# Optimization experiments

Hardware: AMD Instinct MI355X
Metric: run time of the kernel (lower is better)

Reference implementation:

```python
import jax, jax.numpy as jnp
import numpy as np

WS = 8            # window size
N = WS * WS       # tokens per window
C = 192           # in_features
H = 6             # heads
HD = C // H       # head dim
MH = 256          # meta network hidden
BW = 4096         # batch_size * windows
NW_MASK = 64      # number of mask window patterns


def _relative_coords_log():
    idx = np.arange(WS)
    coords = np.stack(np.meshgrid(idx, idx, indexing='ij'), axis=0).reshape(2, -1)  # [2, N]
    rel = coords[:, :, None] - coords[:, None, :]            # [2, N, N]
    rel = rel.transpose(1, 2, 0).reshape(-1, 2).astype(np.float32)  # [N*N, 2]
    return jnp.asarray(np.sign(rel) * np.log1p(np.abs(rel)))


def setup_inputs() -> dict:
    key = jax.random.key(0)
    ks = jax.random.split(key, 12)
    s = 0.02
    return {
        'x': jax.random.normal(ks[0], (BW, C, WS, WS), jnp.float32),
        'mask': jax.random.normal(ks[1], (NW_MASK, N, N), jnp.float32),
        'W_qkv': jax.random.normal(ks[2], (C, 3 * C), jnp.float32) * s,
        'b_qkv': jnp.zeros((3 * C,), jnp.float32),
        'W_proj': jax.random.normal(ks[3], (C, C), jnp.float32) * s,
        'b_proj': jnp.zeros((C,), jnp.float32),
        'mW1': jax.random.normal(ks[4], (2, MH), jnp.float32) * 0.1,
        'mb1': jnp.zeros((MH,), jnp.float32),
        'mW2': jax.random.normal(ks[5], (MH, H), jnp.float32) * 0.1,
        'mb2': jnp.zeros((H,), jnp.float32),
        'tau': jnp.ones((H,), jnp.float32),
    }


def _l2norm(v):
    n = jnp.sqrt(jnp.sum(v * v, axis=-1, keepdims=True))
    return v / jnp.maximum(n, 1e-12)


def reference(x, mask, W_qkv, b_qkv, W_proj, b_proj, mW1, mb1, mW2, mb2, tau):
    Bw = x.shape[0]
    # [Bw, C, ws, ws] -> tokens [Bw, N, C]
    tokens = x.reshape(Bw, C, N).transpose(0, 2, 1)
    qkv = tokens @ W_qkv + b_qkv                                  # [Bw, N, 3C]
    qkv = qkv.reshape(Bw, N, 3, H, HD).transpose(2, 0, 3, 1, 4)   # [3, Bw, H, N, HD]
    q, k, v = qkv[0], qkv[1], qkv[2]
    # scaled cosine attention
    attn = jnp.einsum('bhnd,bhmd->bhnm', _l2norm(q), _l2norm(k))
    attn = attn / jnp.clip(tau, 0.01, None)[None, :, None, None]
    # continuous relative position bias via meta network
    rel_log = _relative_coords_log()                              # [N*N, 2]
    bias = jax.nn.relu(rel_log @ mW1 + mb1) @ mW2 + mb2           # [N*N, H]
    bias = bias.T.reshape(H, N, N)
    attn = attn + bias[None]
    # shifted-window mask, pattern indexed by window id modulo nW_mask
    idx = jnp.arange(Bw) % mask.shape[0]
    attn = attn + mask[idx][:, None]                              # [Bw, 1, N, N]
    attn = jax.nn.softmax(attn, axis=-1)
    out = jnp.einsum('bhnm,bhmd->bhnd', attn, v)
    out = out.transpose(0, 2, 1, 3).reshape(Bw, N, C)
    out = out @ W_proj + b_proj
    # back to [Bw, C, ws, ws]
    return out.transpose(0, 2, 1).reshape(Bw, C, WS, WS)
```

## Files before the change

### kernel.cpp

```cpp
#include <hip/hip_runtime.h>

typedef _Float16 f16;
typedef _Float16 f16x2 __attribute__((ext_vector_type(2)));
typedef _Float16 f16x4 __attribute__((ext_vector_type(4)));
typedef _Float16 f16x8 __attribute__((ext_vector_type(8)));
typedef float f32x4 __attribute__((ext_vector_type(4)));

#define NT 64
#define CH 192
#define NH 6
#define MH 256
#define BWIN 4096
#define LOG2E 1.44269504f

#define STOK 200
#define SMEM_FUSED 49152
#define SMEM_SPLIT 25600

#define MFMA16(a, b, c) __builtin_amdgcn_mfma_f32_16x16x16f16(a, b, c, 0, 0, 0)
#define MFMA32(a, b, c) __builtin_amdgcn_mfma_f32_16x16x32_f16(a, b, c, 0, 0, 0)

__device__ __forceinline__ int qkidx(int n, int d) {
    return n * 32 + ((((d >> 3) + (n >> 1)) & 3) << 3) + (d & 7);
}

__global__ void bias_kernel(const float* __restrict__ mW1, const float* __restrict__ mb1,
                            const float* __restrict__ mW2, const float* __restrict__ mb2,
                            float* __restrict__ bias_tbl) {
    int p = blockIdx.x * blockDim.x + threadIdx.x;
    if (p >= NT * NT) return;
    int n = p >> 6, m = p & 63;
    float di = (float)((n >> 3) - (m >> 3));
    float dj = (float)((n & 7) - (m & 7));
    float r0 = copysignf(log1pf(fabsf(di)), di);
    float r1 = copysignf(log1pf(fabsf(dj)), dj);
    float acc[NH];
#pragma unroll
    for (int h = 0; h < NH; h++) acc[h] = mb2[h];
    for (int k = 0; k < MH; k++) {
        float hv = fmaxf(r0 * mW1[k] + r1 * mW1[MH + k] + mb1[k], 0.0f);
#pragma unroll
        for (int h = 0; h < NH; h++) acc[h] += hv * mW2[k * NH + h];
    }
#pragma unroll
    for (int h = 0; h < NH; h++) bias_tbl[h * (NT * NT) + p] = acc[h];
}

__global__ void prep_kernel(const float* __restrict__ Wqkv, const float* __restrict__ Wproj,
                            f16* __restrict__ Wpk, f16* __restrict__ Wpp) {
    int i = blockIdx.x * blockDim.x + threadIdx.x;
    const int NQ = 36 * 6 * 64 * 8;
    if (i < NQ) {
        int t = i & 7, lane = (i >> 3) & 63, ks = (i >> 9) % 6, ct = i >> 9; ct /= 6;
        int o = 16 * ct + (lane & 15);
        int c = ks * 32 + (lane >> 4) * 8 + t;
        Wpk[i] = (f16)Wqkv[c * 576 + o];
    } else if (i < NQ + 12 * 6 * 64 * 8) {
        int j = i - NQ;
        int t = j & 7, lane = (j >> 3) & 63, ks = (j >> 9) % 6, ct = j >> 9; ct /= 6;
        int o = 16 * ct + (lane & 15);
        int c = ks * 32 + (lane >> 4) * 8 + t;
        Wpp[j] = (f16)Wproj[c * 192 + o];
    }
}

__global__ void comb_kernel(const float* __restrict__ mask, const float* __restrict__ bias_tbl,
                            float* __restrict__ comb) {
    int j = blockIdx.x * blockDim.x + threadIdx.x;
    if (j >= 64 * NH * NT * NT) return;
    int im = j / (NH * NT * NT);
    int rem = j % (NH * NT * NT);
    int h = rem >> 12;
    int p = rem & 4095;
    comb[j] = (mask[im * 4096 + p] + bias_tbl[h * 4096 + p]) * LOG2E;
}

__launch_bounds__(384)
__global__ void qkv_kernel(const float* __restrict__ x, const float* __restrict__ bqkv,
                           const f16* __restrict__ Wpk, f16* __restrict__ qkv_ws) {
    __shared__ __align__(16) f16 tok[NT * STOK];

    const int tid = threadIdx.x;
    const int l   = tid & 63;
    const int w   = __builtin_amdgcn_readfirstlane(tid >> 6);
    const int b   = blockIdx.x;
    const int c16 = l & 15;
    const int g4  = l >> 4;

    {
        const float* xb = x + (size_t)b * (CH * NT);
        const int n4 = 4 * c16;
#pragma unroll
        for (int i = 0; i < 4; i++) {
            int c = 32 * w + 8 * g4 + 2 * i;
            f32x4 a0 = *(const f32x4*)(xb + c * NT + n4);
            f32x4 a1 = *(const f32x4*)(xb + (c + 1) * NT + n4);
#pragma unroll
            for (int j = 0; j < 4; j++) {
                f16x2 p;
                p[0] = (f16)a0[j];
                p[1] = (f16)a1[j];
                *(f16x2*)(tok + (n4 + j) * STOK + c) = p;
            }
        }
    }
    __syncthreads();

    f16* dstq = qkv_ws + (size_t)(b * NH + w) * 6144;
    f16* dstk = dstq + 2048;
    f16* dstv = dstq + 4096;

    {
        f32x4 acc[2][4] = {};
#pragma unroll
        for (int ks = 0; ks < 6; ks++) {
            f16x8 af[4];
#pragma unroll
            for (int nt = 0; nt < 4; nt++)
                af[nt] = *(const f16x8*)(tok + (16 * nt + c16) * STOK + ks * 32 + 8 * g4);
#pragma unroll
            for (int dt = 0; dt < 2; dt++) {
                f16x8 wf = *(const f16x8*)(Wpk + (((size_t)(2 * w + dt) * 6 + ks) * 64 + l) * 8);
#pragma unroll
                for (int nt = 0; nt < 4; nt++)
                    acc[dt][nt] = MFMA32(wf, af[nt], acc[dt][nt]);
            }
        }
        f32x4 bb0 = *(const f32x4*)(bqkv + 32 * w + 4 * g4);
        f32x4 bb1 = *(const f32x4*)(bqkv + 32 * w + 16 + 4 * g4);
#pragma unroll
        for (int nt = 0; nt < 4; nt++) {
            float a0[4], a1[4];
            float ss = 0.f;
#pragma unroll
            for (int r = 0; r < 4; r++) {
                a0[r] = acc[0][nt][r] + bb0[r];
                a1[r] = acc[1][nt][r] + bb1[r];
                ss += a0[r] * a0[r] + a1[r] * a1[r];
            }
            ss += __shfl_xor(ss, 16);
            ss += __shfl_xor(ss, 32);
            float inv = 1.0f / fmaxf(sqrtf(ss), 1e-12f);
            f16x4 h0, h1;
#pragma unroll
            for (int r = 0; r < 4; r++) {
                h0[r] = (f16)(a0[r] * inv);
                h1[r] = (f16)(a1[r] * inv);
            }
            *(f16x4*)(dstq + (16 * nt + c16) * 32 + 4 * g4)      = h0;
            *(f16x4*)(dstq + (16 * nt + c16) * 32 + 16 + 4 * g4) = h1;
        }
    }
    {
        f32x4 acc[2][4] = {};
#pragma unroll
        for (int ks = 0; ks < 6; ks++) {
            f16x8 af[4];
#pragma unroll
            for (int nt = 0; nt < 4; nt++)
                af[nt] = *(const f16x8*)(tok + (16 * nt + c16) * STOK + ks * 32 + 8 * g4);
#pragma unroll
            for (int dt = 0; dt < 2; dt++) {
                f16x8 wf = *(const f16x8*)(Wpk + (((size_t)(12 + 2 * w + dt) * 6 + ks) * 64 + l) * 8);
#pragma unroll
                for (int nt = 0; nt < 4; nt++)
                    acc[dt][nt] = MFMA32(wf, af[nt], acc[dt][nt]);
            }
        }
        f32x4 bb0 = *(const f32x4*)(bqkv + CH + 32 * w + 4 * g4);
        f32x4 bb1 = *(const f32x4*)(bqkv + CH + 32 * w + 16 + 4 * g4);
#pragma unroll
        for (int nt = 0; nt < 4; nt++) {
            float a0[4], a1[4];
            float ss = 0.f;
#pragma unroll
            for (int r = 0; r < 4; r++) {
                a0[r] = acc[0][nt][r] + bb0[r];
                a1[r] = acc[1][nt][r] + bb1[r];
                ss += a0[r] * a0[r] + a1[r] * a1[r];
            }
            ss += __shfl_xor(ss, 16);
            ss += __shfl_xor(ss, 32);
            float inv = 1.0f / fmaxf(sqrtf(ss), 1e-12f);
            f16x4 h0, h1;
#pragma unroll
            for (int r = 0; r < 4; r++) {
                h0[r] = (f16)(a0[r] * inv);
                h1[r] = (f16)(a1[r] * inv);
            }
            *(f16x4*)(dstk + (16 * nt + c16) * 32 + 4 * g4)      = h0;
            *(f16x4*)(dstk + (16 * nt + c16) * 32 + 16 + 4 * g4) = h1;
        }
    }
    {
        f32x4 acc[2][4] = {};
#pragma unroll
        for (int ks = 0; ks < 6; ks++) {
            f16x8 af[4];
#pragma unroll
            for (int mt = 0; mt < 4; mt++)
                af[mt] = *(const f16x8*)(tok + (16 * mt + c16) * STOK + ks * 32 + 8 * g4);
#pragma unroll
            for (int dt = 0; dt < 2; dt++) {
                f16x8 wf = *(const f16x8*)(Wpk + (((size_t)(24 + 2 * w + dt) * 6 + ks) * 64 + l) * 8);
#pragma unroll
                for (int mt = 0; mt < 4; mt++)
                    acc[dt][mt] = MFMA32(af[mt], wf, acc[dt][mt]);
            }
        }
#pragma unroll
        for (int dt = 0; dt < 2; dt++) {
            float bb = bqkv[384 + 32 * w + 16 * dt + c16];
#pragma unroll
            for (int mt = 0; mt < 4; mt++) {
                f16x4 h;
#pragma unroll
                for (int r = 0; r < 4; r++) h[r] = (f16)(acc[dt][mt][r] + bb);
                *(f16x4*)(dstv + ((dt * 4 + mt) * 64 + l) * 4) = h;
            }
        }
    }
}

__launch_bounds__(384)
__global__ void attn2_kernel(const float* __restrict__ tau, const f16* __restrict__ Wpp,
                             const float* __restrict__ bproj, const float* __restrict__ comb,
                             const f16* __restrict__ qkv_ws, float* __restrict__ out) {
    __shared__ __align__(16) f16 ao[NT * STOK];

    const int tid = threadIdx.x;
    const int l   = tid & 63;
    const int w   = __builtin_amdgcn_readfirstlane(tid >> 6);
    const int b   = blockIdx.x;
    const int c16 = l & 15;
    const int g4  = l >> 4;

    const f16* qg = qkv_ws + (size_t)(b * NH + w) * 6144;
    const f16* kg = qg + 2048;
    const f16* vg = qg + 4096;

    f16x4 vb[2][4];
#pragma unroll
    for (int dt = 0; dt < 2; dt++)
#pragma unroll
        for (int mk = 0; mk < 4; mk++)
            vb[dt][mk] = *(const f16x4*)(vg + ((dt * 4 + mk) * 64 + l) * 4);

    const float itau_l2 = LOG2E / fmaxf(tau[w], 0.01f);
    const float* cb = comb + ((size_t)((b & 63) * NH + w)) * (NT * NT);

#pragma unroll
    for (int half = 0; half < 2; half++) {
        f16x8 aqf[2];
#pragma unroll
        for (int ntl = 0; ntl < 2; ntl++)
            aqf[ntl] = *(const f16x8*)(qg + (16 * (2 * half + ntl) + c16) * 32 + 8 * g4);
        f32x4 sv[4][2];
#pragma unroll
        for (int mt = 0; mt < 4; mt++) {
            f16x8 akf = *(const f16x8*)(kg + (16 * mt + c16) * 32 + 8 * g4);
#pragma unroll
            for (int ntl = 0; ntl < 2; ntl++) {
                f32x4 z = {};
                sv[mt][ntl] = MFMA32(akf, aqf[ntl], z);
            }
        }
#pragma unroll
        for (int mt = 0; mt < 4; mt++)
#pragma unroll
            for (int ntl = 0; ntl < 2; ntl++) {
                int nt = 2 * half + ntl;
                f32x4 cc = *(const f32x4*)(cb + (16 * nt + c16) * NT + 16 * mt + 4 * g4);
#pragma unroll
                for (int r = 0; r < 4; r++)
                    sv[mt][ntl][r] = sv[mt][ntl][r] * itau_l2 + cc[r];
            }
#pragma unroll
        for (int ntl = 0; ntl < 2; ntl++) {
            float mx = sv[0][ntl][0];
#pragma unroll
            for (int mt = 0; mt < 4; mt++)
#pragma unroll
                for (int r = 0; r < 4; r++) mx = fmaxf(mx, sv[mt][ntl][r]);
            mx = fmaxf(mx, __shfl_xor(mx, 16));
            mx = fmaxf(mx, __shfl_xor(mx, 32));
            float sum = 0.f;
#pragma unroll
            for (int mt = 0; mt < 4; mt++)
#pragma unroll
                for (int r = 0; r < 4; r++) {
                    float p = exp2f(sv[mt][ntl][r] - mx);
                    sv[mt][ntl][r] = p;
                    sum += p;
                }
            sum += __shfl_xor(sum, 16);
            sum += __shfl_xor(sum, 32);
            float ris = 1.0f / sum;
#pragma unroll
            for (int mt = 0; mt < 4; mt++)
#pragma unroll
                for (int r = 0; r < 4; r++) sv[mt][ntl][r] *= ris;
        }
        f16x4 pa[4][2];
#pragma unroll
        for (int mk = 0; mk < 4; mk++)
#pragma unroll
            for (int ntl = 0; ntl < 2; ntl++) {
                f16x4 h;
#pragma unroll
                for (int r = 0; r < 4; r++) h[r] = (f16)sv[mk][ntl][r];
                pa[mk][ntl] = h;
            }
        f32x4 av[2][2] = {};
#pragma unroll
        for (int mk = 0; mk < 4; mk++)
#pragma unroll
            for (int ntl = 0; ntl < 2; ntl++)
#pragma unroll
                for (int dt = 0; dt < 2; dt++)
                    av[ntl][dt] = MFMA16(pa[mk][ntl], vb[dt][mk], av[ntl][dt]);
#pragma unroll
        for (int ntl = 0; ntl < 2; ntl++)
#pragma unroll
            for (int dt = 0; dt < 2; dt++)
#pragma unroll
                for (int r = 0; r < 4; r++)
                    ao[(16 * (2 * half + ntl) + 4 * g4 + r) * STOK + 32 * w + 16 * dt + c16] =
                        (f16)av[ntl][dt][r];
    }
    __syncthreads();

    f32x4 acc2[2][4] = {};
#pragma unroll
    for (int ks = 0; ks < 6; ks++) {
        f16x8 af[4];
#pragma unroll
        for (int rt = 0; rt < 4; rt++)
            af[rt] = *(const f16x8*)(ao + (16 * rt + c16) * STOK + ks * 32 + 8 * g4);
#pragma unroll
        for (int c2 = 0; c2 < 2; c2++) {
            f16x8 bw = *(const f16x8*)(Wpp + (((size_t)(2 * w + c2) * 6 + ks) * 64 + l) * 8);
#pragma unroll
            for (int rt = 0; rt < 4; rt++)
                acc2[c2][rt] = MFMA32(af[rt], bw, acc2[c2][rt]);
        }
    }
    float* ob = out + (size_t)b * (CH * NT);
#pragma unroll
    for (int c2 = 0; c2 < 2; c2++) {
        int c = 16 * (2 * w + c2) + c16;
        float bp = bproj[c];
#pragma unroll
        for (int rt = 0; rt < 4; rt++) {
            f32x4 o4 = acc2[c2][rt];
            o4[0] += bp; o4[1] += bp; o4[2] += bp; o4[3] += bp;
            *(f32x4*)(ob + c * NT + 16 * rt + 4 * g4) = o4;
        }
    }
}

__launch_bounds__(384)
__global__ void attn_fused_kernel(const float* __restrict__ x, const float* __restrict__ bqkv,
                                  const float* __restrict__ bproj, const float* __restrict__ tau,
                                  const f16* __restrict__ Wpk, const f16* __restrict__ Wpp,
                                  const float* __restrict__ comb, float* __restrict__ out) {
    __shared__ __align__(16) char smem[SMEM_FUSED];
    f16* tok = (f16*)smem;
    f16* qk  = (f16*)smem;
    f16* ao  = (f16*)smem;

    const int b   = blockIdx.x;
    const int tid = threadIdx.x;
    const int l   = tid & 63;
    const int w   = __builtin_amdgcn_readfirstlane(tid >> 6);
    const int c16 = l & 15;
    const int g4  = l >> 4;

    {
        const float* xb = x + (size_t)b * (CH * NT);
        const int n4 = 4 * c16;
#pragma unroll
        for (int i = 0; i < 4; i++) {
            int c = 32 * w + 8 * g4 + 2 * i;
            f32x4 a0 = *(const f32x4*)(xb + c * NT + n4);
            f32x4 a1 = *(const f32x4*)(xb + (c + 1) * NT + n4);
#pragma unroll
            for (int j = 0; j < 4; j++) {
                f16x2 p;
                p[0] = (f16)a0[j];
                p[1] = (f16)a1[j];
                *(f16x2*)(tok + (n4 + j) * STOK + c) = p;
            }
        }
    }
    __syncthreads();

    f16x4 hq[2][4], hk[2][4];
    {
        f32x4 aq_[2][4] = {};
#pragma unroll
        for (int ks = 0; ks < 6; ks++) {
            f16x8 af[4];
#pragma unroll
            for (int nt = 0; nt < 4; nt++)
                af[nt] = *(const f16x8*)(tok + (16 * nt + c16) * STOK + ks * 32 + 8 * g4);
#pragma unroll
            for (int dt = 0; dt < 2; dt++) {
                f16x8 wf = *(const f16x8*)(Wpk + (((size_t)(2 * w + dt) * 6 + ks) * 64 + l) * 8);
#pragma unroll
                for (int nt = 0; nt < 4; nt++)
                    aq_[dt][nt] = MFMA32(wf, af[nt], aq_[dt][nt]);
            }
        }
#pragma unroll
        for (int dt = 0; dt < 2; dt++) {
            f32x4 bb = *(const f32x4*)(bqkv + 32 * w + 16 * dt + 4 * g4);
#pragma unroll
            for (int nt = 0; nt < 4; nt++)
#pragma unroll
                for (int r = 0; r < 4; r++) aq_[dt][nt][r] += bb[r];
        }
#pragma unroll
        for (int nt = 0; nt < 4; nt++) {
            float ss = 0.f;
#pragma unroll
            for (int dt = 0; dt < 2; dt++)
#pragma unroll
                for (int r = 0; r < 4; r++) ss += aq_[dt][nt][r] * aq_[dt][nt][r];
            ss += __shfl_xor(ss, 16);
            ss += __shfl_xor(ss, 32);
            float iq = 1.0f / fmaxf(sqrtf(ss), 1e-12f);
#pragma unroll
            for (int dt = 0; dt < 2; dt++)
#pragma unroll
                for (int r = 0; r < 4; r++) hq[dt][nt][r] = (f16)(aq_[dt][nt][r] * iq);
        }
    }
    {
        f32x4 ak_[2][4] = {};
#pragma unroll
        for (int ks = 0; ks < 6; ks++) {
            f16x8 af[4];
#pragma unroll
            for (int nt = 0; nt < 4; nt++)
                af[nt] = *(const f16x8*)(tok + (16 * nt + c16) * STOK + ks * 32 + 8 * g4);
#pragma unroll
            for (int dt = 0; dt < 2; dt++) {
                f16x8 wf = *(const f16x8*)(Wpk + (((size_t)(12 + 2 * w + dt) * 6 + ks) * 64 + l) * 8);
#pragma unroll
                for (int nt = 0; nt < 4; nt++)
                    ak_[dt][nt] = MFMA32(wf, af[nt], ak_[dt][nt]);
            }
        }
#pragma unroll
        for (int dt = 0; dt < 2; dt++) {
            f32x4 bb = *(const f32x4*)(bqkv + 192 + 32 * w + 16 * dt + 4 * g4);
#pragma unroll
            for (int nt = 0; nt < 4; nt++)
#pragma unroll
                for (int r = 0; r < 4; r++) ak_[dt][nt][r] += bb[r];
        }
#pragma unroll
        for (int nt = 0; nt < 4; nt++) {
            float ss = 0.f;
#pragma unroll
            for (int dt = 0; dt < 2; dt++)
#pragma unroll
                for (int r = 0; r < 4; r++) ss += ak_[dt][nt][r] * ak_[dt][nt][r];
            ss += __shfl_xor(ss, 16);
            ss += __shfl_xor(ss, 32);
            float ik = 1.0f / fmaxf(sqrtf(ss), 1e-12f);
#pragma unroll
            for (int dt = 0; dt < 2; dt++)
#pragma unroll
                for (int r = 0; r < 4; r++) hk[dt][nt][r] = (f16)(ak_[dt][nt][r] * ik);
        }
    }
    f16x4 vb[2][4];
    {
        f32x4 av_[2][4] = {};
#pragma unroll
        for (int ks = 0; ks < 6; ks++) {
            f16x8 af[4];
#pragma unroll
            for (int mt = 0; mt < 4; mt++)
                af[mt] = *(const f16x8*)(tok + (16 * mt + c16) * STOK + ks * 32 + 8 * g4);
#pragma unroll
            for (int dt = 0; dt < 2; dt++) {
                f16x8 wf = *(const f16x8*)(Wpk + (((size_t)(24 + 2 * w + dt) * 6 + ks) * 64 + l) * 8);
#pragma unroll
                for (int mt = 0; mt < 4; mt++)
                    av_[dt][mt] = MFMA32(af[mt], wf, av_[dt][mt]);
            }
        }
#pragma unroll
        for (int dt = 0; dt < 2; dt++) {
            float bb = bqkv[384 + 32 * w + 16 * dt + c16];
#pragma unroll
            for (int mt = 0; mt < 4; mt++)
#pragma unroll
                for (int r = 0; r < 4; r++) vb[dt][mt][r] = (f16)(av_[dt][mt][r] + bb);
        }
    }
    __syncthreads();

    f16* qh = qk + (w * 2 + 0) * 2048;
    f16* kh = qk + (w * 2 + 1) * 2048;
#pragma unroll
    for (int nt = 0; nt < 4; nt++)
#pragma unroll
        for (int dt = 0; dt < 2; dt++) {
            int base = qkidx(16 * nt + c16, 16 * dt + 4 * g4);
            *(f16x2*)(qh + base)     = f16x2{hq[dt][nt][0], hq[dt][nt][1]};
            *(f16x2*)(qh + base + 2) = f16x2{hq[dt][nt][2], hq[dt][nt][3]};
            *(f16x2*)(kh + base)     = f16x2{hk[dt][nt][0], hk[dt][nt][1]};
            *(f16x2*)(kh + base + 2) = f16x2{hk[dt][nt][2], hk[dt][nt][3]};
        }

    f32x4 sv[4][4];
    {
        f16x8 aqf[4];
#pragma unroll
        for (int t = 0; t < 4; t++)
            aqf[t] = *(const f16x8*)(qh + qkidx(16 * t + c16, 8 * g4));
#pragma unroll
        for (int mt = 0; mt < 4; mt++) {
            f16x8 akf = *(const f16x8*)(kh + qkidx(16 * mt + c16, 8 * g4));
#pragma unroll
            for (int nt = 0; nt < 4; nt++) {
                f32x4 z = {};
                sv[mt][nt] = MFMA32(akf, aqf[nt], z);
            }
        }
    }
    {
        const float itau_l2 = LOG2E / fmaxf(tau[w], 0.01f);
        const float* cb = comb + ((size_t)((b & 63) * NH + w)) * (NT * NT);
#pragma unroll
        for (int mt = 0; mt < 4; mt++)
#pragma unroll
            for (int nt = 0; nt < 4; nt++) {
                f32x4 cc = *(const f32x4*)(cb + (16 * nt + c16) * NT + 16 * mt + 4 * g4);
#pragma unroll
                for (int r = 0; r < 4; r++)
                    sv[mt][nt][r] = sv[mt][nt][r] * itau_l2 + cc[r];
            }
    }
#pragma unroll
    for (int nt = 0; nt < 4; nt++) {
        float mx = sv[0][nt][0];
#pragma unroll
        for (int mt = 0; mt < 4; mt++)
#pragma unroll
            for (int r = 0; r < 4; r++) mx = fmaxf(mx, sv[mt][nt][r]);
        mx = fmaxf(mx, __shfl_xor(mx, 16));
        mx = fmaxf(mx, __shfl_xor(mx, 32));
        float sum = 0.f;
#pragma unroll
        for (int mt = 0; mt < 4; mt++)
#pragma unroll
            for (int r = 0; r < 4; r++) {
                float p = exp2f(sv[mt][nt][r] - mx);
                sv[mt][nt][r] = p;
                sum += p;
            }
        sum += __shfl_xor(sum, 16);
        sum += __shfl_xor(sum, 32);
        float ris = 1.0f / sum;
#pragma unroll
        for (int mt = 0; mt < 4; mt++)
#pragma unroll
            for (int r = 0; r < 4; r++) sv[mt][nt][r] *= ris;
    }
    f16x4 pa[4][4];
#pragma unroll
    for (int mk = 0; mk < 4; mk++)
#pragma unroll
        for (int nt = 0; nt < 4; nt++) {
            f16x4 h;
#pragma unroll
            for (int r = 0; r < 4; r++) h[r] = (f16)sv[mk][nt][r];
            pa[mk][nt] = h;
        }
    f32x4 av[4][2] = {};
#pragma unroll
    for (int mk = 0; mk < 4; mk++)
#pragma unroll
        for (int nt = 0; nt < 4; nt++)
#pragma unroll
            for (int dt = 0; dt < 2; dt++)
                av[nt][dt] = MFMA16(pa[mk][nt], vb[dt][mk], av[nt][dt]);

    __syncthreads();
#pragma unroll
    for (int nt = 0; nt < 4; nt++)
#pragma unroll
        for (int dt = 0; dt < 2; dt++)
#pragma unroll
            for (int r = 0; r < 4; r++)
                ao[(16 * nt + 4 * g4 + r) * STOK + 32 * w + 16 * dt + c16] = (f16)av[nt][dt][r];
    __syncthreads();

    f32x4 acc2[2][4] = {};
#pragma unroll
    for (int ks = 0; ks < 6; ks++) {
        f16x8 af[4];
#pragma unroll
        for (int rt = 0; rt < 4; rt++)
            af[rt] = *(const f16x8*)(ao + (16 * rt + c16) * STOK + ks * 32 + 8 * g4);
#pragma unroll
        for (int c2 = 0; c2 < 2; c2++) {
            f16x8 bw = *(const f16x8*)(Wpp + (((size_t)(2 * w + c2) * 6 + ks) * 64 + l) * 8);
#pragma unroll
            for (int rt = 0; rt < 4; rt++)
                acc2[c2][rt] = MFMA32(af[rt], bw, acc2[c2][rt]);
        }
    }
    float* ob = out + (size_t)b * (CH * NT);
#pragma unroll
    for (int c2 = 0; c2 < 2; c2++) {
        int c = 16 * (2 * w + c2) + c16;
        float bp = bproj[c];
#pragma unroll
        for (int rt = 0; rt < 4; rt++) {
            f32x4 o4 = acc2[c2][rt];
            o4[0] += bp; o4[1] += bp; o4[2] += bp; o4[3] += bp;
            *(f32x4*)(ob + c * NT + 16 * rt + 4 * g4) = o4;
        }
    }
}

#define WS_BIAS 0
#define WS_WPK  98304
#define WS_WPP  319488
#define WS_COMB 393216
#define WS_QKV  6684672
#define WS_NEED ((size_t)WS_QKV + (size_t)BWIN * NH * 6144 * 2)

extern "C" void kernel_launch(void* const* d_in, const int* in_sizes, int n_in,
                              void* d_out, int out_size, void* d_ws, size_t ws_size,
                              hipStream_t stream) {
    const float* x     = (const float*)d_in[0];
    const float* mask  = (const float*)d_in[1];
    const float* Wqkv  = (const float*)d_in[2];
    const float* bqkv  = (const float*)d_in[3];
    const float* Wproj = (const float*)d_in[4];
    const float* bproj = (const float*)d_in[5];
    const float* mW1   = (const float*)d_in[6];
    const float* mb1   = (const float*)d_in[7];
    const float* mW2   = (const float*)d_in[8];
    const float* mb2   = (const float*)d_in[9];
    const float* tau   = (const float*)d_in[10];

    char* ws = (char*)d_ws;
    float* bias_tbl = (float*)(ws + WS_BIAS);
    f16*   Wpk      = (f16*)(ws + WS_WPK);
    f16*   Wpp      = (f16*)(ws + WS_WPP);
    float* comb     = (float*)(ws + WS_COMB);
    f16*   qkv_ws   = (f16*)(ws + WS_QKV);

    bias_kernel<<<16, 256, 0, stream>>>(mW1, mb1, mW2, mb2, bias_tbl);
    int prep_n = 36 * 6 * 64 * 8 + 12 * 6 * 64 * 8;
    prep_kernel<<<(prep_n + 255) / 256, 256, 0, stream>>>(Wqkv, Wproj, Wpk, Wpp);
    int comb_n = 64 * NH * NT * NT;
    comb_kernel<<<(comb_n + 255) / 256, 256, 0, stream>>>(mask, bias_tbl, comb);

    if (ws_size >= WS_NEED) {
        qkv_kernel<<<BWIN, 384, 0, stream>>>(x, bqkv, Wpk, qkv_ws);
        attn2_kernel<<<BWIN, 384, 0, stream>>>(tau, Wpp, bproj, comb, qkv_ws, (float*)d_out);
    } else {
        attn_fused_kernel<<<BWIN, 384, 0, stream>>>(x, bqkv, bproj, tau, Wpk, Wpp, comb,
                                                    (float*)d_out);
    }
}
```

Baseline: 330.3 us.

## Hoist all global weight, QKV and bias loads up front into registers

In the QKV kernel, all 36 weight fragments per wave are now fetched with inline-asm global loads before the token transpose, then a single vmcnt wait follows. In the attention kernel, Q, K, V and the full 64x64 combined bias tile are loaded up front so the two halves of the score computation merge into one pass. V is also written and read as 16-byte vectors instead of 8-byte ones. This trades many more live VGPRs (launch_bounds set to one block per SIMD) for fewer serialized load latencies, at the risk of lower occupancy or spills.

Result: slower. 409.9 us (+24.1%).

```diff
diff --git a/kernel.cpp b/kernel.cpp
--- a/kernel.cpp
+++ b/kernel.cpp
@@ -15,10 +15,22 @@
 
 #define STOK 200
 #define SMEM_FUSED 49152
-#define SMEM_SPLIT 25600
 
 #define MFMA16(a, b, c) __builtin_amdgcn_mfma_f32_16x16x16f16(a, b, c, 0, 0, 0)
 #define MFMA32(a, b, c) __builtin_amdgcn_mfma_f32_16x16x32_f16(a, b, c, 0, 0, 0)
+
+__device__ __forceinline__ f16x8 gld16(const f16* p) {
+    f16x8 r;
+    asm volatile("global_load_dwordx4 %0, %1, off" : "=v"(r) : "v"(p));
+    return r;
+}
+__device__ __forceinline__ f32x4 gldf4(const float* p) {
+    f32x4 r;
+    asm volatile("global_load_dwordx4 %0, %1, off" : "=v"(r) : "v"(p));
+    return r;
+}
+#define WAIT_VMCNT0() do { asm volatile("s_waitcnt vmcnt(0)" ::: "memory"); \
+                           __builtin_amdgcn_sched_barrier(0); } while (0)
 
 __device__ __forceinline__ int qkidx(int n, int d) {
     return n * 32 + ((((d >> 3) + (n >> 1)) & 3) << 3) + (d & 7);
@@ -75,7 +87,35 @@
     comb[j] = (mask[im * 4096 + p] + bias_tbl[h * 4096 + p]) * LOG2E;
 }
 
-__launch_bounds__(384)
+__device__ __forceinline__ void norm_store(const f32x4 (&acc)[2][4], const float* __restrict__ bq,
+                                           int c16, int g4, f16* __restrict__ dst) {
+    f32x4 bb0 = *(const f32x4*)(bq + 4 * g4);
+    f32x4 bb1 = *(const f32x4*)(bq + 16 + 4 * g4);
+#pragma unroll
+    for (int nt = 0; nt < 4; nt++) {
+        float a0[4], a1[4];
+        float ss = 0.f;
+#pragma unroll
+        for (int r = 0; r < 4; r++) {
+            a0[r] = acc[0][nt][r] + bb0[r];
+            a1[r] = acc[1][nt][r] + bb1[r];
+            ss += a0[r] * a0[r] + a1[r] * a1[r];
+        }
+        ss += __shfl_xor(ss, 16);
+        ss += __shfl_xor(ss, 32);
+        float inv = 1.0f / fmaxf(sqrtf(ss), 1e-12f);
+        f16x4 h0, h1;
+#pragma unroll
+        for (int r = 0; r < 4; r++) {
+            h0[r] = (f16)(a0[r] * inv);
+            h1[r] = (f16)(a1[r] * inv);
+        }
+        *(f16x4*)(dst + (16 * nt + c16) * 32 + 4 * g4)      = h0;
+        *(f16x4*)(dst + (16 * nt + c16) * 32 + 16 + 4 * g4) = h1;
+    }
+}
+
+__launch_bounds__(384, 1)
 __global__ void qkv_kernel(const float* __restrict__ x, const float* __restrict__ bqkv,
                            const f16* __restrict__ Wpk, f16* __restrict__ qkv_ws) {
     __shared__ __align__(16) f16 tok[NT * STOK];
@@ -87,6 +127,16 @@
     const int c16 = l & 15;
     const int g4  = l >> 4;
 
+    f16x8 wfq[6][2], wfk[6][2], wfv[6][2];
+#pragma unroll
+    for (int ks = 0; ks < 6; ks++)
+#pragma unroll
+        for (int dt = 0; dt < 2; dt++) {
+            wfq[ks][dt] = gld16(Wpk + (((size_t)(2 * w + dt) * 6 + ks) * 64 + l) * 8);
+            wfk[ks][dt] = gld16(Wpk + (((size_t)(12 + 2 * w + dt) * 6 + ks) * 64 + l) * 8);
+            wfv[ks][dt] = gld16(Wpk + (((size_t)(24 + 2 * w + dt) * 6 + ks) * 64 + l) * 8);
+        }
+
     {
         const float* xb = x + (size_t)b * (CH * NT);
         const int n4 = 4 * c16;
@@ -105,6 +155,7 @@
         }
     }
     __syncthreads();
+    WAIT_VMCNT0();
 
     f16* dstq = qkv_ws + (size_t)(b * NH + w) * 6144;
     f16* dstk = dstq + 2048;
@@ -119,37 +170,12 @@
             for (int nt = 0; nt < 4; nt++)
                 af[nt] = *(const f16x8*)(tok + (16 * nt + c16) * STOK + ks * 32 + 8 * g4);
 #pragma unroll
-            for (int dt = 0; dt < 2; dt++) {
-                f16x8 wf = *(const f16x8*)(Wpk + (((size_t)(2 * w + dt) * 6 + ks) * 64 + l) * 8);
+            for (int dt = 0; dt < 2; dt++)
 #pragma unroll
                 for (int nt = 0; nt < 4; nt++)
-                    acc[dt][nt] = MFMA32(wf, af[nt], acc[dt][nt]);
-            }
-        }
-        f32x4 bb0 = *(const f32x4*)(bqkv + 32 * w + 4 * g4);
-        f32x4 bb1 = *(const f32x4*)(bqkv + 32 * w + 16 + 4 * g4);
-#pragma unroll
-        for (int nt = 0; nt < 4; nt++) {
-            float a0[4], a1[4];
-            float ss = 0.f;
-#pragma unroll
-            for (int r = 0; r < 4; r++) {
-                a0[r] = acc[0][nt][r] + bb0[r];
-                a1[r] = acc[1][nt][r] + bb1[r];
-                ss += a0[r] * a0[r] + a1[r] * a1[r];
-            }
-            ss += __shfl_xor(ss, 16);
-            ss += __shfl_xor(ss, 32);
-            float inv = 1.0f / fmaxf(sqrtf(ss), 1e-12f);
-            f16x4 h0, h1;
-#pragma unroll
-            for (int r = 0; r < 4; r++) {
-                h0[r] = (f16)(a0[r] * inv);
-                h1[r] = (f16)(a1[r] * inv);
-            }
-            *(f16x4*)(dstq + (16 * nt + c16) * 32 + 4 * g4)      = h0;
-            *(f16x4*)(dstq + (16 * nt + c16) * 32 + 16 + 4 * g4) = h1;
-        }
+                    acc[dt][nt] = MFMA32(wfq[ks][dt], af[nt], acc[dt][nt]);
+        }
+        norm_store(acc, bqkv + 32 * w, c16, g4, dstq);
     }
     {
         f32x4 acc[2][4] = {};
@@ -160,37 +186,12 @@
             for (int nt = 0; nt < 4; nt++)
                 af[nt] = *(const f16x8*)(tok + (16 * nt + c16) * STOK + ks * 32 + 8 * g4);
 #pragma unroll
-            for (int dt = 0; dt < 2; dt++) {
-                f16x8 wf = *(const f16x8*)(Wpk + (((size_t)(12 + 2 * w + dt) * 6 + ks) * 64 + l) * 8);
+            for (int dt = 0; dt < 2; dt++)
 #pragma unroll
                 for (int nt = 0; nt < 4; nt++)
-                    acc[dt][nt] = MFMA32(wf, af[nt], acc[dt][nt]);
-            }
-        }
-        f32x4 bb0 = *(const f32x4*)(bqkv + CH + 32 * w + 4 * g4);
-        f32x4 bb1 = *(const f32x4*)(bqkv + CH + 32 * w + 16 + 4 * g4);
-#pragma unroll
-        for (int nt = 0; nt < 4; nt++) {
-            float a0[4], a1[4];
-            float ss = 0.f;
-#pragma unroll
-            for (int r = 0; r < 4; r++) {
-                a0[r] = acc[0][nt][r] + bb0[r];
-                a1[r] = acc[1][nt][r] + bb1[r];
-                ss += a0[r] * a0[r] + a1[r] * a1[r];
-            }
-            ss += __shfl_xor(ss, 16);
-            ss += __shfl_xor(ss, 32);
-            float inv = 1.0f / fmaxf(sqrtf(ss), 1e-12f);
-            f16x4 h0, h1;
-#pragma unroll
-            for (int r = 0; r < 4; r++) {
-                h0[r] = (f16)(a0[r] * inv);
-                h1[r] = (f16)(a1[r] * inv);
-            }
-            *(f16x4*)(dstk + (16 * nt + c16) * 32 + 4 * g4)      = h0;
-            *(f16x4*)(dstk + (16 * nt + c16) * 32 + 16 + 4 * g4) = h1;
-        }
+                    acc[dt][nt] = MFMA32(wfk[ks][dt], af[nt], acc[dt][nt]);
+        }
+        norm_store(acc, bqkv + CH + 32 * w, c16, g4, dstk);
     }
     {
         f32x4 acc[2][4] = {};
@@ -201,28 +202,32 @@
             for (int mt = 0; mt < 4; mt++)
                 af[mt] = *(const f16x8*)(tok + (16 * mt + c16) * STOK + ks * 32 + 8 * g4);
 #pragma unroll
-            for (int dt = 0; dt < 2; dt++) {
-                f16x8 wf = *(const f16x8*)(Wpk + (((size_t)(24 + 2 * w + dt) * 6 + ks) * 64 + l) * 8);
+            for (int dt = 0; dt < 2; dt++)
 #pragma unroll
                 for (int mt = 0; mt < 4; mt++)
-                    acc[dt][mt] = MFMA32(af[mt], wf, acc[dt][mt]);
-            }
-        }
+                    acc[dt][mt] = MFMA32(af[mt], wfv[ks][dt], acc[dt][mt]);
+        }
+        f16x4 hv[2][4];
 #pragma unroll
         for (int dt = 0; dt < 2; dt++) {
             float bb = bqkv[384 + 32 * w + 16 * dt + c16];
 #pragma unroll
-            for (int mt = 0; mt < 4; mt++) {
-                f16x4 h;
-#pragma unroll
-                for (int r = 0; r < 4; r++) h[r] = (f16)(acc[dt][mt][r] + bb);
-                *(f16x4*)(dstv + ((dt * 4 + mt) * 64 + l) * 4) = h;
-            }
-        }
-    }
-}
-
-__launch_bounds__(384)
+            for (int mt = 0; mt < 4; mt++)
+#pragma unroll
+                for (int r = 0; r < 4; r++) hv[dt][mt][r] = (f16)(acc[dt][mt][r] + bb);
+        }
+#pragma unroll
+        for (int p = 0; p < 4; p++) {
+            int dt = p >> 1, m0 = 2 * (p & 1);
+            f16x8 v8;
+#pragma unroll
+            for (int r = 0; r < 4; r++) { v8[r] = hv[dt][m0][r]; v8[4 + r] = hv[dt][m0 + 1][r]; }
+            *(f16x8*)(dstv + (p * 64 + l) * 8) = v8;
+        }
+    }
+}
+
+__launch_bounds__(384, 1)
 __global__ void attn2_kernel(const float* __restrict__ tau, const f16* __restrict__ Wpp,
                              const float* __restrict__ bproj, const float* __restrict__ comb,
                              const f16* __restrict__ qkv_ws, float* __restrict__ out) {
@@ -236,98 +241,105 @@
     const int g4  = l >> 4;
 
     const f16* qg = qkv_ws + (size_t)(b * NH + w) * 6144;
-    const f16* kg = qg + 2048;
-    const f16* vg = qg + 4096;
+    const float* cb = comb + ((size_t)((b & 63) * NH + w)) * (NT * NT);
+
+    f16x8 qf[4], kf[4], vf[4];
+    f32x4 cc[4][4];
+#pragma unroll
+    for (int nt = 0; nt < 4; nt++)
+        qf[nt] = gld16(qg + (16 * nt + c16) * 32 + 8 * g4);
+#pragma unroll
+    for (int mt = 0; mt < 4; mt++)
+        kf[mt] = gld16(qg + 2048 + (16 * mt + c16) * 32 + 8 * g4);
+#pragma unroll
+    for (int p = 0; p < 4; p++)
+        vf[p] = gld16(qg + 4096 + (p * 64 + l) * 8);
+#pragma unroll
+    for (int mt = 0; mt < 4; mt++)
+#pragma unroll
+        for (int nt = 0; nt < 4; nt++)
+            cc[mt][nt] = gldf4(cb + (16 * nt + c16) * NT + 16 * mt + 4 * g4);
+
+    const float itau_l2 = LOG2E / fmaxf(tau[w], 0.01f);
+    WAIT_VMCNT0();
 
     f16x4 vb[2][4];
 #pragma unroll
-    for (int dt = 0; dt < 2; dt++)
-#pragma unroll
-        for (int mk = 0; mk < 4; mk++)
-            vb[dt][mk] = *(const f16x4*)(vg + ((dt * 4 + mk) * 64 + l) * 4);
-
-    const float itau_l2 = LOG2E / fmaxf(tau[w], 0.01f);
-    const float* cb = comb + ((size_t)((b & 63) * NH + w)) * (NT * NT);
-
-#pragma unroll
-    for (int half = 0; half < 2; half++) {
-        f16x8 aqf[2];
-#pragma unroll
-        for (int ntl = 0; ntl < 2; ntl++)
-            aqf[ntl] = *(const f16x8*)(qg + (16 * (2 * half + ntl) + c16) * 32 + 8 * g4);
-        f32x4 sv[4][2];
-#pragma unroll
-        for (int mt = 0; mt < 4; mt++) {
-            f16x8 akf = *(const f16x8*)(kg + (16 * mt + c16) * 32 + 8 * g4);
-#pragma unroll
-            for (int ntl = 0; ntl < 2; ntl++) {
-                f32x4 z = {};
-                sv[mt][ntl] = MFMA32(akf, aqf[ntl], z);
-            }
-        }
+    for (int p = 0; p < 4; p++) {
+        int dt = p >> 1, m0 = 2 * (p & 1);
+#pragma unroll
+        for (int r = 0; r < 4; r++) { vb[dt][m0][r] = vf[p][r]; vb[dt][m0 + 1][r] = vf[p][4 + r]; }
+    }
+
+    f32x4 sv[4][4];
+#pragma unroll
+    for (int mt = 0; mt < 4; mt++)
+#pragma unroll
+        for (int nt = 0; nt < 4; nt++) {
+            f32x4 z = {};
+            sv[mt][nt] = MFMA32(kf[mt], qf[nt], z);
+        }
+#pragma unroll
+    for (int mt = 0; mt < 4; mt++)
+#pragma unroll
+        for (int nt = 0; nt < 4; nt++)
+#pragma unroll
+            for (int r = 0; r < 4; r++)
+                sv[mt][nt][r] = sv[mt][nt][r] * itau_l2 + cc[mt][nt][r];
+
+#pragma unroll
+    for (int nt = 0; nt < 4; nt++) {
+        float mx = sv[0][nt][0];
 #pragma unroll
         for (int mt = 0; mt < 4; mt++)
 #pragma unroll
-            for (int ntl = 0; ntl < 2; ntl++) {
-                int nt = 2 * half + ntl;
-                f32x4 cc = *(const f32x4*)(cb + (16 * nt + c16) * NT + 16 * mt + 4 * g4);
-#pragma unroll
-                for (int r = 0; r < 4; r++)
-                    sv[mt][ntl][r] = sv[mt][ntl][r] * itau_l2 + cc[r];
-            }
-#pragma unroll
-        for (int ntl = 0; ntl < 2; ntl++) {
-            float mx = sv[0][ntl][0];
-#pragma unroll
-            for (int mt = 0; mt < 4; mt++)
-#pragma unroll
-                for (int r = 0; r < 4; r++) mx = fmaxf(mx, sv[mt][ntl][r]);
-            mx = fmaxf(mx, __shfl_xor(mx, 16));
-            mx = fmaxf(mx, __shfl_xor(mx, 32));
-            float sum = 0.f;
-#pragma unroll
-            for (int mt = 0; mt < 4; mt++)
-#pragma unroll
-                for (int r = 0; r < 4; r++) {
-                    float p = exp2f(sv[mt][ntl][r] - mx);
-                    sv[mt][ntl][r] = p;
-                    sum += p;
-                }
-            sum += __shfl_xor(sum, 16);
-            sum += __shfl_xor(sum, 32);
-            float ris = 1.0f / sum;
-#pragma unroll
-            for (int mt = 0; mt < 4; mt++)
-#pragma unroll
-                for (int r = 0; r < 4; r++) sv[mt][ntl][r] *= ris;
-        }
-        f16x4 pa[4][2];
-#pragma unroll
-        for (int mk = 0; mk < 4; mk++)
-#pragma unroll
-            for (int ntl = 0; ntl < 2; ntl++) {
-                f16x4 h;
-#pragma unroll
-                for (int r = 0; r < 4; r++) h[r] = (f16)sv[mk][ntl][r];
-                pa[mk][ntl] = h;
-            }
-        f32x4 av[2][2] = {};
-#pragma unroll
-        for (int mk = 0; mk < 4; mk++)
-#pragma unroll
-            for (int ntl = 0; ntl < 2; ntl++)
-#pragma unroll
-                for (int dt = 0; dt < 2; dt++)
-                    av[ntl][dt] = MFMA16(pa[mk][ntl], vb[dt][mk], av[ntl][dt]);
-#pragma unroll
-        for (int ntl = 0; ntl < 2; ntl++)
-#pragma unroll
-            for (int dt = 0; dt < 2; dt++)
-#pragma unroll
-                for (int r = 0; r < 4; r++)
-                    ao[(16 * (2 * half + ntl) + 4 * g4 + r) * STOK + 32 * w + 16 * dt + c16] =
-                        (f16)av[ntl][dt][r];
-    }
+            for (int r = 0; r < 4; r++) mx = fmaxf(mx, sv[mt][nt][r]);
+        mx = fmaxf(mx, __shfl_xor(mx, 16));
+        mx = fmaxf(mx, __shfl_xor(mx, 32));
+        float sum = 0.f;
+#pragma unroll
+        for (int mt = 0; mt < 4; mt++)
+#pragma unroll
+            for (int r = 0; r < 4; r++) {
+                float p = exp2f(sv[mt][nt][r] - mx);
+                sv[mt][nt][r] = p;
+                sum += p;
+            }
+        sum += __shfl_xor(sum, 16);
+        sum += __shfl_xor(sum, 32);
+        float ris = 1.0f / sum;
+#pragma unroll
+        for (int mt = 0; mt < 4; mt++)
+#pragma unroll
+            for (int r = 0; r < 4; r++) sv[mt][nt][r] *= ris;
+    }
+
+    f16x4 pa[4][4];
+#pragma unroll
+    for (int mk = 0; mk < 4; mk++)
+#pragma unroll
+        for (int nt = 0; nt < 4; nt++) {
+            f16x4 h;
+#pragma unroll
+            for (int r = 0; r < 4; r++) h[r] = (f16)sv[mk][nt][r];
+            pa[mk][nt] = h;
+        }
+    f32x4 av[4][2] = {};
+#pragma unroll
+    for (int mk = 0; mk < 4; mk++)
+#pragma unroll
+        for (int nt = 0; nt < 4; nt++)
+#pragma unroll
+            for (int dt = 0; dt < 2; dt++)
+                av[nt][dt] = MFMA16(pa[mk][nt], vb[dt][mk], av[nt][dt]);
+
+#pragma unroll
+    for (int nt = 0; nt < 4; nt++)
+#pragma unroll
+        for (int dt = 0; dt < 2; dt++)
+#pragma unroll
+            for (int r = 0; r < 4; r++)
+                ao[(16 * nt + 4 * g4 + r) * STOK + 32 * w + 16 * dt + c16] = (f16)av[nt][dt][r];
     __syncthreads();
 
     f32x4 acc2[2][4] = {};
```
